# Performance work log

Hardware: AMD Instinct MI355X
Metric: run time of the kernel (lower is better)

The kernel has to match this reference:

```python
import jax, jax.numpy as jnp
import numpy as np

B, N, DIM, H, DH = 32, 1024, 512, 8, 64
SCALE = DH ** -0.5


def setup_inputs() -> dict:
    key = jax.random.key(0)
    k1, k2, k3, k4 = jax.random.split(key, 4)
    x = jax.random.normal(k1, (B, N, DIM), dtype=jnp.float32)
    W_qkv = jax.random.normal(k2, (DIM, 3 * H * DH), dtype=jnp.float32) * (DIM ** -0.5)
    W_out = jax.random.normal(k3, (H * DH, DIM), dtype=jnp.float32) * ((H * DH) ** -0.5)
    b_out = jnp.zeros((DIM,), dtype=jnp.float32)
    decay_mask = jax.random.uniform(k4, (1, H, N, N), dtype=jnp.float32)
    return {"x": x, "W_qkv": W_qkv, "W_out": W_out, "b_out": b_out,
            "decay_mask": decay_mask}


def reference(x, W_qkv, W_out, b_out, decay_mask):
    b, n, _ = x.shape
    qkv = x @ W_qkv                                  # [b, n, 3*h*d]
    q, k, v = jnp.split(qkv, 3, axis=-1)
    reshape = lambda t: t.reshape(b, n, H, DH).transpose(0, 2, 1, 3)  # b h n d
    q, k, v = reshape(q), reshape(k), reshape(v)
    dots = jnp.einsum('bhid,bhjd->bhij', q, k) * SCALE
    attn = jax.nn.softmax(dots, axis=-1)
    attn = attn * decay_mask                          # post-softmax decay mask
    out = jnp.einsum('bhij,bhjd->bhid', attn, v)      # [b, h, n, d]
    out = out.transpose(0, 2, 1, 3).reshape(b, n, H * DH)
    return out @ W_out + b_out
```

## Files before the change

### kernel.cpp

```cpp
#include <hip/hip_runtime.h>
#include <hip/hip_fp16.h>
#include <math.h>

#define Bb 32
#define Nn 1024
#define DIMc 512
#define Hh 8
#define DHd 64
#define GK 512

typedef __attribute__((ext_vector_type(8))) short short8;
typedef __attribute__((ext_vector_type(8))) _Float16 half8;
typedef __attribute__((ext_vector_type(2))) __fp16 fp16x2;
typedef __attribute__((ext_vector_type(4))) float floatx4;

#define MFMA16 __builtin_amdgcn_mfma_f32_16x16x32_f16

#if __has_builtin(__builtin_amdgcn_exp2f)
#define EXP2(x) __builtin_amdgcn_exp2f(x)
#else
#define EXP2(x) __expf((x) * 0.6931471805599453f)
#endif

__device__ __forceinline__ unsigned short f16_bits(float f) {
    return __half_as_ushort(__float2half(f));
}
__device__ __forceinline__ int cvt_pk_f16(float a, float b) {
    fp16x2 r = __builtin_amdgcn_cvt_pkrtz(a, b);
    return __builtin_bit_cast(int, r);
}

__global__ __launch_bounds__(256) void transpose_half_kernel(
    const float* __restrict__ src, int K, int N,
    unsigned short* __restrict__ dh)
{
    __shared__ float T[32][33];
    const int tid = threadIdx.x;
    const int c = tid & 31, r0 = tid >> 5;
    const int nb = blockIdx.x * 32, kb = blockIdx.y * 32;
    #pragma unroll
    for (int i = 0; i < 4; ++i)
        T[r0 + i * 8][c] = src[(size_t)(kb + r0 + i * 8) * N + nb + c];
    __syncthreads();
    #pragma unroll
    for (int i = 0; i < 4; ++i) {
        int n = r0 + i * 8;
        dh[(size_t)(nb + n) * K + kb + c] = f16_bits(T[c][n]);
    }
}

__global__ __launch_bounds__(256) void decay_to_half_kernel(
    const float* __restrict__ D, unsigned short* __restrict__ D16)
{
    size_t i = ((size_t)blockIdx.x * 256 + threadIdx.x) * 4;
    float4 v = *(const float4*)(D + i);
    ushort4 o;
    o.x = f16_bits(v.x * 0.00390625f);
    o.y = f16_bits(v.y * 0.00390625f);
    o.z = f16_bits(v.z * 0.00390625f);
    o.w = f16_bits(v.w * 0.00390625f);
    *(ushort4*)(D16 + i) = o;
}

__global__ __launch_bounds__(256) void x_to_half_kernel(
    const float* __restrict__ X, unsigned short* __restrict__ Xf)
{
    size_t i = ((size_t)blockIdx.x * 256 + threadIdx.x) * 8;
    float4 a = *(const float4*)(X + i);
    float4 b = *(const float4*)(X + i + 4);
    float f[8] = {a.x, a.y, a.z, a.w, b.x, b.y, b.z, b.w};
    short8 o;
    #pragma unroll
    for (int e = 0; e < 8; ++e) o[e] = (short)f16_bits(f[e]);
    *(short8*)(Xf + i) = o;
}

__device__ __forceinline__ void gload_lds16(const unsigned short* g, unsigned short* l) {
    __builtin_amdgcn_global_load_lds(
        (const __attribute__((address_space(1))) unsigned int*)g,
        (__attribute__((address_space(3))) unsigned int*)l,
        16, 0, 0);
}

#define STAGE2(PA, PB, k0s, bufp) do {                                         \
    _Pragma("unroll")                                                          \
    for (int i_ = 0; i_ < 2; ++i_) {                                           \
        const int row_ = i_ * 64 + w * 16 + l16;                               \
        const size_t aoff_ = (size_t)(m0 + row_) * GK + (k0s) + quad * 8;      \
        const size_t boff_ = (size_t)(n0 + row_) * GK + (k0s) + quad * 8;      \
        const int lbe_ = (i_ * 4 + w) * 512;                                   \
        gload_lds16((PA) + aoff_, (bufp) + lbe_);                              \
        gload_lds16((PB) + boff_, (bufp) + 4096 + lbe_);                       \
    }                                                                          \
} while (0)

__global__ __launch_bounds__(256) void gemm_qkv_mfma(
    const unsigned short* __restrict__ Xf, const unsigned short* __restrict__ Wf,
    unsigned short* __restrict__ Qf, unsigned short* __restrict__ Kf,
    unsigned short* __restrict__ Vt)
{
    __shared__ union {
        unsigned short buf[3][8192];
        unsigned short bounce[128][136];
    } u;

    const int tid  = threadIdx.x;
    const int w    = tid >> 6;
    const int lane = tid & 63;
    const int quad = lane >> 4;
    const int l16  = lane & 15;
    const int lb = blockIdx.x;
    const int wg = (lb & 7) * 384 + (lb >> 3);
    const int n0 = (wg % 12) * 128;
    const int m0 = (wg / 12) * 128;
    const int wm = w >> 1, wn = w & 1;

    floatx4 acc[4][4];
    #pragma unroll
    for (int im = 0; im < 4; ++im)
        #pragma unroll
        for (int in = 0; in < 4; ++in)
            acc[im][in] = (floatx4){0.f, 0.f, 0.f, 0.f};

    STAGE2(Xf, Wf, 0, u.buf[0]);
    STAGE2(Xf, Wf, 32, u.buf[1]);

    int rd = 0;
    for (int k0 = 0; k0 < GK; k0 += 32) {
        asm volatile("s_waitcnt vmcnt(4) lgkmcnt(0)" ::: "memory");
        __builtin_amdgcn_s_barrier();
        __builtin_amdgcn_sched_barrier(0);
        const int wr = (rd >= 1) ? rd - 1 : 2;
        STAGE2(Xf, Wf, k0 + 64, u.buf[wr]);

        const unsigned short* rp = u.buf[rd];
        half8 faf[4], fbf[4];
        #pragma unroll
        for (int t = 0; t < 4; ++t) {
            const int ca = ((wm * 4 + t) * 4 + quad) * 16 + l16;
            faf[t] = *(const half8*)&rp[ca * 8];
            const int cb = ((wn * 4 + t) * 4 + quad) * 16 + l16;
            fbf[t] = *(const half8*)&rp[4096 + cb * 8];
        }
        #pragma unroll
        for (int im = 0; im < 4; ++im)
            #pragma unroll
            for (int in = 0; in < 4; ++in)
                acc[im][in] = MFMA16(faf[im], fbf[in], acc[im][in], 0, 0, 0);
        rd = (rd == 2) ? 0 : rd + 1;
    }
    asm volatile("s_waitcnt vmcnt(0)" ::: "memory");

    const int which = n0 >> 9;
    const int b    = m0 >> 10;
    const int tokb = m0 & 1023;
    if (which < 2) {
        unsigned short* OUT = which ? Kf : Qf;
        const float sc = which ? 1.0f : 0.18033688011112042f;
        #pragma unroll
        for (int im = 0; im < 4; ++im) {
            const int tok = tokb + wm * 64 + im * 16 + quad * 4;
            #pragma unroll
            for (int in = 0; in < 4; ++in) {
                const int ncol = n0 + wn * 64 + in * 16 + l16;
                const int h = (ncol & 511) >> 6, d = ncol & 63;
                const size_t base = ((size_t)(b * Hh + h) * Nn + tok) * DHd + d;
                #pragma unroll
                for (int r = 0; r < 4; ++r)
                    OUT[base + (size_t)r * DHd] = f16_bits(acc[im][in][r] * sc);
            }
        }
    } else {
        __syncthreads();
        #pragma unroll
        for (int im = 0; im < 4; ++im)
            #pragma unroll
            for (int in = 0; in < 4; ++in)
                #pragma unroll
                for (int r = 0; r < 4; ++r)
                    u.bounce[wm * 64 + im * 16 + quad * 4 + r][wn * 64 + in * 16 + l16] =
                        f16_bits(acc[im][in][r]);
        __syncthreads();
        const int c = tid >> 1, tq = (tid & 1) * 64;
        const int h = ((n0 + c) & 511) >> 6, d = c & 63;
        unsigned short* vbase = Vt + ((size_t)(b * Hh + h) * DHd + d) * Nn + tokb;
        #pragma unroll
        for (int uu = 0; uu < 8; ++uu) {
            short8 v8;
            #pragma unroll
            for (int e = 0; e < 8; ++e)
                v8[e] = (short)u.bounce[tq + uu * 8 + e][c];
            *(short8*)&vbase[tq + uu * 8] = v8;
        }
    }
}

__global__ __launch_bounds__(256) void attn_mfma_kernel(
    const unsigned short* __restrict__ Qf, const unsigned short* __restrict__ Kf,
    const unsigned short* __restrict__ Vt, const unsigned short* __restrict__ D16,
    unsigned short* __restrict__ AOf)
{
    __shared__ unsigned short Kfs[2][32][72];
    __shared__ unsigned short Vts[2][64][40];

    const int tid  = threadIdx.x;
    const int wave = tid >> 6;
    const int lane = tid & 63;
    const int quad = lane >> 4;
    const int l16  = lane & 15;
    const int lb   = blockIdx.x;
    const int xcd  = lb & 7;
    const int r_   = lb >> 3;
    const int h    = r_ >> 5;
    const int rem  = r_ & 31;
    const int i0   = (rem >> 2) << 7;
    const int b    = xcd * 4 + (rem & 3);
    const int bh   = b * 8 + h;
    const int iw   = i0 + wave * 32;

    const size_t qoffA = ((size_t)bh * Nn + iw + l16) * DHd + quad * 8;
    const size_t qoffB = qoffA + (size_t)16 * DHd;
    const half8 qA0 = *(const half8*)(Qf + qoffA);
    const half8 qA1 = *(const half8*)(Qf + qoffA + 32);
    const half8 qB0 = *(const half8*)(Qf + qoffB);
    const half8 qB1 = *(const half8*)(Qf + qoffB + 32);

    floatx4 oA[4], oB[4];
    #pragma unroll
    for (int nt = 0; nt < 4; ++nt) {
        oA[nt] = (floatx4){0.f, 0.f, 0.f, 0.f};
        oB[nt] = (floatx4){0.f, 0.f, 0.f, 0.f};
    }
    float lA = 0.f, lB = 0.f;

    const int sj  = tid >> 3, sc2 = (tid & 7) * 8;
    const int prow = ((sj >> 2) & 1) * 16 + ((sj >> 3) << 2) + (sj & 3);
    const int vd  = tid >> 2, vj8 = (tid & 3) * 8;
    const unsigned short* DpA = D16 + ((size_t)h * Nn + iw + l16) * Nn + quad * 8;
    const unsigned short* DpB = DpA + (size_t)16 * Nn;

    const unsigned short* kpf = Kf + (size_t)bh * Nn * DHd + (size_t)sj * DHd + sc2;
    const unsigned short* vpv = Vt + (size_t)bh * DHd * Nn + (size_t)vd * Nn + vj8;

    short8 pk_f = *(const short8*)kpf; kpf += 32 * DHd;
    short8 pk_v = *(const short8*)vpv; vpv += 32;
    *(short8*)&Kfs[0][prow][sc2] = pk_f;
    *(short8*)&Vts[0][vd][vj8]   = pk_v;
    __syncthreads();

    int cur = 0;
    for (int j0 = 0; j0 < Nn; j0 += 32) {
        pk_f = *(const short8*)kpf; kpf += 32 * DHd;
        pk_v = *(const short8*)vpv; vpv += 32;
        const short8 dcA = *(const short8*)(DpA + j0);
        const short8 dcB = *(const short8*)(DpB + j0);

        floatx4 sA[2], sB[2];
        #pragma unroll
        for (int nh = 0; nh < 2; ++nh) {
            const int kr = nh * 16 + l16;
            half8 kf0 = *(const half8*)&Kfs[cur][kr][quad * 8];
            half8 kf1 = *(const half8*)&Kfs[cur][kr][32 + quad * 8];
            floatx4 a = (floatx4){0.f, 0.f, 0.f, 0.f};
            a = MFMA16(kf0, qA0, a, 0, 0, 0);
            a = MFMA16(kf1, qA1, a, 0, 0, 0);
            sA[nh] = a;
            floatx4 c = (floatx4){0.f, 0.f, 0.f, 0.f};
            c = MFMA16(kf0, qB0, c, 0, 0, 0);
            c = MFMA16(kf1, qB1, c, 0, 0, 0);
            sB[nh] = c;
        }

        float pA[8], pB[8];
        #pragma unroll
        for (int e = 0; e < 4; ++e) {
            pA[e]     = EXP2(sA[0][e]);
            pA[4 + e] = EXP2(sA[1][e]);
            pB[e]     = EXP2(sB[0][e]);
            pB[4 + e] = EXP2(sB[1][e]);
        }
        lA += ((pA[0] + pA[1]) + (pA[2] + pA[3])) + ((pA[4] + pA[5]) + (pA[6] + pA[7]));
        lB += ((pB[0] + pB[1]) + (pB[2] + pB[3])) + ((pB[4] + pB[5]) + (pB[6] + pB[7]));

        union { int i4[4]; half8 v8; } pfA, pfB;
        const int* dA = (const int*)&dcA;
        const int* dB = (const int*)&dcB;
        #pragma unroll
        for (int e = 0; e < 4; ++e) {
            fp16x2 pa = __builtin_bit_cast(fp16x2, cvt_pk_f16(pA[2 * e], pA[2 * e + 1]));
            fp16x2 da = __builtin_bit_cast(fp16x2, dA[e]);
            pfA.i4[e] = __builtin_bit_cast(int, pa * da);
            fp16x2 pb = __builtin_bit_cast(fp16x2, cvt_pk_f16(pB[2 * e], pB[2 * e + 1]));
            fp16x2 db = __builtin_bit_cast(fp16x2, dB[e]);
            pfB.i4[e] = __builtin_bit_cast(int, pb * db);
        }
        #pragma unroll
        for (int nt = 0; nt < 4; ++nt) {
            half8 vf = *(const half8*)&Vts[cur][nt * 16 + l16][quad * 8];
            oA[nt] = MFMA16(pfA.v8, vf, oA[nt], 0, 0, 0);
            oB[nt] = MFMA16(pfB.v8, vf, oB[nt], 0, 0, 0);
        }

        *(short8*)&Kfs[cur ^ 1][prow][sc2] = pk_f;
        *(short8*)&Vts[cur ^ 1][vd][vj8]   = pk_v;
        __syncthreads();
        cur ^= 1;
    }

    float lsA = lA;
    lsA += __shfl_xor(lsA, 16);
    lsA += __shfl_xor(lsA, 32);
    float lsB = lB;
    lsB += __shfl_xor(lsB, 16);
    lsB += __shfl_xor(lsB, 32);
    const float invA = 256.f / lsA;
    const float invB = 256.f / lsB;
    float irA[4], irB[4];
    #pragma unroll
    for (int r = 0; r < 4; ++r) {
        irA[r] = __shfl(invA, quad * 4 + r);
        irB[r] = __shfl(invB, quad * 4 + r);
    }
    const size_t aobA = ((size_t)b * Nn + iw) * DIMc + h * DHd;
    const size_t aobB = aobA + (size_t)16 * DIMc;
    #pragma unroll
    for (int nt = 0; nt < 4; ++nt)
        #pragma unroll
        for (int r = 0; r < 4; ++r) {
            const size_t ro = (size_t)(quad * 4 + r) * DIMc + nt * 16 + l16;
            AOf[aobA + ro] = f16_bits(oA[nt][r] * irA[r]);
            AOf[aobB + ro] = f16_bits(oB[nt][r] * irB[r]);
        }
}

__global__ __launch_bounds__(256) void gemm_out_mfma(
    const unsigned short* __restrict__ Af, const unsigned short* __restrict__ Wf,
    const float* __restrict__ bias, float* __restrict__ C)
{
    __shared__ unsigned short sbuf[3][8192];

    const int tid  = threadIdx.x;
    const int w    = tid >> 6;
    const int lane = tid & 63;
    const int quad = lane >> 4;
    const int l16  = lane & 15;
    const int lb = blockIdx.x;
    const int wg = (lb & 7) * 128 + (lb >> 3);
    const int n0 = (wg & 3) * 128;
    const int m0 = (wg >> 2) * 128;
    const int wm = w >> 1, wn = w & 1;

    floatx4 acc[4][4];
    #pragma unroll
    for (int im = 0; im < 4; ++im)
        #pragma unroll
        for (int in = 0; in < 4; ++in)
            acc[im][in] = (floatx4){0.f, 0.f, 0.f, 0.f};

    STAGE2(Af, Wf, 0, sbuf[0]);
    STAGE2(Af, Wf, 32, sbuf[1]);

    int rd = 0;
    for (int k0 = 0; k0 < GK; k0 += 32) {
        asm volatile("s_waitcnt vmcnt(4) lgkmcnt(0)" ::: "memory");
        __builtin_amdgcn_s_barrier();
        __builtin_amdgcn_sched_barrier(0);
        const int wr = (rd >= 1) ? rd - 1 : 2;
        STAGE2(Af, Wf, k0 + 64, sbuf[wr]);

        const unsigned short* rp = sbuf[rd];
        half8 faf[4], fbf[4];
        #pragma unroll
        for (int t = 0; t < 4; ++t) {
            const int ca = ((wm * 4 + t) * 4 + quad) * 16 + l16;
            faf[t] = *(const half8*)&rp[ca * 8];
            const int cb = ((wn * 4 + t) * 4 + quad) * 16 + l16;
            fbf[t] = *(const half8*)&rp[4096 + cb * 8];
        }
        #pragma unroll
        for (int im = 0; im < 4; ++im)
            #pragma unroll
            for (int in = 0; in < 4; ++in)
                acc[im][in] = MFMA16(faf[im], fbf[in], acc[im][in], 0, 0, 0);
        rd = (rd == 2) ? 0 : rd + 1;
    }
    asm volatile("s_waitcnt vmcnt(0)" ::: "memory");

    float biasv[4];
    #pragma unroll
    for (int in = 0; in < 4; ++in) biasv[in] = bias[n0 + wn * 64 + in * 16 + l16];
    #pragma unroll
    for (int im = 0; im < 4; ++im)
        #pragma unroll
        for (int in = 0; in < 4; ++in) {
            const int mrow = m0 + wm * 64 + im * 16 + quad * 4;
            const int ncol = n0 + wn * 64 + in * 16 + l16;
            #pragma unroll
            for (int r = 0; r < 4; ++r)
                C[(size_t)(mrow + r) * DIMc + ncol] = acc[im][in][r] + biasv[in];
        }
}

extern "C" void kernel_launch(void* const* d_in, const int* in_sizes, int n_in,
                              void* d_out, int out_size, void* d_ws, size_t ws_size,
                              hipStream_t stream)
{
    const float* x     = (const float*)d_in[0];
    const float* Wqkv  = (const float*)d_in[1];
    const float* Wout  = (const float*)d_in[2];
    const float* bout  = (const float*)d_in[3];
    const float* decay = (const float*)d_in[4];

    const size_t E = (size_t)32768 * 512;
    unsigned short* p = (unsigned short*)d_ws;
    unsigned short* Qf  = p; p += E;
    unsigned short* Kf  = p; p += E;
    unsigned short* Vt  = p; p += E;
    unsigned short* AOf = p; p += E;
    unsigned short* Wq  = p; p += 786432;
    unsigned short* Wo  = p; p += 262144;
    unsigned short* D16 = p;
    unsigned short* Xf = AOf;

    transpose_half_kernel<<<dim3(48, 16), 256, 0, stream>>>(Wqkv, 512, 1536, Wq);
    transpose_half_kernel<<<dim3(16, 16), 256, 0, stream>>>(Wout, 512, 512, Wo);
    decay_to_half_kernel<<<dim3(8192), 256, 0, stream>>>(decay, D16);
    x_to_half_kernel<<<dim3(8192), 256, 0, stream>>>(x, Xf);
    gemm_qkv_mfma<<<dim3(3072), 256, 0, stream>>>(Xf, Wq, Qf, Kf, Vt);
    attn_mfma_kernel<<<dim3(2048), 256, 0, stream>>>(Qf, Kf, Vt, D16, AOf);
    gemm_out_mfma<<<dim3(1024), 256, 0, stream>>>(AOf, Wo, bout, (float*)d_out);
}
```

Measured before the change: 293.7 us.

## Load GEMM operands straight from global memory into registers, bypassing LDS staging

Both MFMA GEMMs (the QKV projection and the output projection) drop the triple-buffered global-to-LDS staging with per-step barriers. Each wave now loads its A and B fragments directly from global memory into registers, double-buffered across two 32-wide K steps. This removes the LDS traffic and the block-wide barriers, frees shared memory (which may raise occupancy), and removes one __syncthreads before the V transpose bounce. In exchange, operand tiles are no longer shared between waves through LDS, so each tile is fetched twice through the caches. The final prefetch also reads 64 elements past the end of the K range, which is unused but goes out of bounds on the last row.

```diff
diff --git a/kernel.cpp b/kernel.cpp
--- a/kernel.cpp
+++ b/kernel.cpp
@@ -75,34 +75,12 @@
     *(short8*)(Xf + i) = o;
 }
 
-__device__ __forceinline__ void gload_lds16(const unsigned short* g, unsigned short* l) {
-    __builtin_amdgcn_global_load_lds(
-        (const __attribute__((address_space(1))) unsigned int*)g,
-        (__attribute__((address_space(3))) unsigned int*)l,
-        16, 0, 0);
-}
-
-#define STAGE2(PA, PB, k0s, bufp) do {                                         \
-    _Pragma("unroll")                                                          \
-    for (int i_ = 0; i_ < 2; ++i_) {                                           \
-        const int row_ = i_ * 64 + w * 16 + l16;                               \
-        const size_t aoff_ = (size_t)(m0 + row_) * GK + (k0s) + quad * 8;      \
-        const size_t boff_ = (size_t)(n0 + row_) * GK + (k0s) + quad * 8;      \
-        const int lbe_ = (i_ * 4 + w) * 512;                                   \
-        gload_lds16((PA) + aoff_, (bufp) + lbe_);                              \
-        gload_lds16((PB) + boff_, (bufp) + 4096 + lbe_);                       \
-    }                                                                          \
-} while (0)
-
 __global__ __launch_bounds__(256) void gemm_qkv_mfma(
     const unsigned short* __restrict__ Xf, const unsigned short* __restrict__ Wf,
     unsigned short* __restrict__ Qf, unsigned short* __restrict__ Kf,
     unsigned short* __restrict__ Vt)
 {
-    __shared__ union {
-        unsigned short buf[3][8192];
-        unsigned short bounce[128][136];
-    } u;
+    __shared__ unsigned short bounce[128][136];
 
     const int tid  = threadIdx.x;
     const int w    = tid >> 6;
@@ -122,34 +100,37 @@
         for (int in = 0; in < 4; ++in)
             acc[im][in] = (floatx4){0.f, 0.f, 0.f, 0.f};
 
-    STAGE2(Xf, Wf, 0, u.buf[0]);
-    STAGE2(Xf, Wf, 32, u.buf[1]);
-
-    int rd = 0;
-    for (int k0 = 0; k0 < GK; k0 += 32) {
-        asm volatile("s_waitcnt vmcnt(4) lgkmcnt(0)" ::: "memory");
-        __builtin_amdgcn_s_barrier();
-        __builtin_amdgcn_sched_barrier(0);
-        const int wr = (rd >= 1) ? rd - 1 : 2;
-        STAGE2(Xf, Wf, k0 + 64, u.buf[wr]);
-
-        const unsigned short* rp = u.buf[rd];
-        half8 faf[4], fbf[4];
+    const unsigned short* ap = Xf + (size_t)(m0 + wm * 64 + l16) * GK + quad * 8;
+    const unsigned short* bp = Wf + (size_t)(n0 + wn * 64 + l16) * GK + quad * 8;
+
+    half8 aC[4], bC[4], aN[4], bN[4];
+    #pragma unroll
+    for (int t = 0; t < 4; ++t) {
+        aC[t] = *(const half8*)(ap + (size_t)t * 16 * GK);
+        bC[t] = *(const half8*)(bp + (size_t)t * 16 * GK);
+    }
+    for (int k0 = 0; k0 < GK; k0 += 64) {
         #pragma unroll
         for (int t = 0; t < 4; ++t) {
-            const int ca = ((wm * 4 + t) * 4 + quad) * 16 + l16;
-            faf[t] = *(const half8*)&rp[ca * 8];
-            const int cb = ((wn * 4 + t) * 4 + quad) * 16 + l16;
-            fbf[t] = *(const half8*)&rp[4096 + cb * 8];
+            aN[t] = *(const half8*)(ap + (size_t)t * 16 * GK + k0 + 32);
+            bN[t] = *(const half8*)(bp + (size_t)t * 16 * GK + k0 + 32);
         }
         #pragma unroll
         for (int im = 0; im < 4; ++im)
             #pragma unroll
             for (int in = 0; in < 4; ++in)
-                acc[im][in] = MFMA16(faf[im], fbf[in], acc[im][in], 0, 0, 0);
-        rd = (rd == 2) ? 0 : rd + 1;
-    }
-    asm volatile("s_waitcnt vmcnt(0)" ::: "memory");
+                acc[im][in] = MFMA16(aC[im], bC[in], acc[im][in], 0, 0, 0);
+        #pragma unroll
+        for (int t = 0; t < 4; ++t) {
+            aC[t] = *(const half8*)(ap + (size_t)t * 16 * GK + k0 + 64);
+            bC[t] = *(const half8*)(bp + (size_t)t * 16 * GK + k0 + 64);
+        }
+        #pragma unroll
+        for (int im = 0; im < 4; ++im)
+            #pragma unroll
+            for (int in = 0; in < 4; ++in)
+                acc[im][in] = MFMA16(aN[im], bN[in], acc[im][in], 0, 0, 0);
+    }
 
     const int which = n0 >> 9;
     const int b    = m0 >> 10;
@@ -171,14 +152,13 @@
             }
         }
     } else {
-        __syncthreads();
         #pragma unroll
         for (int im = 0; im < 4; ++im)
             #pragma unroll
             for (int in = 0; in < 4; ++in)
                 #pragma unroll
                 for (int r = 0; r < 4; ++r)
-                    u.bounce[wm * 64 + im * 16 + quad * 4 + r][wn * 64 + in * 16 + l16] =
+                    bounce[wm * 64 + im * 16 + quad * 4 + r][wn * 64 + in * 16 + l16] =
                         f16_bits(acc[im][in][r]);
         __syncthreads();
         const int c = tid >> 1, tq = (tid & 1) * 64;
@@ -189,7 +169,7 @@
             short8 v8;
             #pragma unroll
             for (int e = 0; e < 8; ++e)
-                v8[e] = (short)u.bounce[tq + uu * 8 + e][c];
+                v8[e] = (short)bounce[tq + uu * 8 + e][c];
             *(short8*)&vbase[tq + uu * 8] = v8;
         }
     }
@@ -337,8 +317,6 @@
     const unsigned short* __restrict__ Af, const unsigned short* __restrict__ Wf,
     const float* __restrict__ bias, float* __restrict__ C)
 {
-    __shared__ unsigned short sbuf[3][8192];
-
     const int tid  = threadIdx.x;
     const int w    = tid >> 6;
     const int lane = tid & 63;
@@ -357,34 +335,37 @@
         for (int in = 0; in < 4; ++in)
             acc[im][in] = (floatx4){0.f, 0.f, 0.f, 0.f};
 
-    STAGE2(Af, Wf, 0, sbuf[0]);
-    STAGE2(Af, Wf, 32, sbuf[1]);
-
-    int rd = 0;
-    for (int k0 = 0; k0 < GK; k0 += 32) {
-        asm volatile("s_waitcnt vmcnt(4) lgkmcnt(0)" ::: "memory");
-        __builtin_amdgcn_s_barrier();
-        __builtin_amdgcn_sched_barrier(0);
-        const int wr = (rd >= 1) ? rd - 1 : 2;
-        STAGE2(Af, Wf, k0 + 64, sbuf[wr]);
-
-        const unsigned short* rp = sbuf[rd];
-        half8 faf[4], fbf[4];
+    const unsigned short* ap = Af + (size_t)(m0 + wm * 64 + l16) * GK + quad * 8;
+    const unsigned short* bp = Wf + (size_t)(n0 + wn * 64 + l16) * GK + quad * 8;
+
+    half8 aC[4], bC[4], aN[4], bN[4];
+    #pragma unroll
+    for (int t = 0; t < 4; ++t) {
+        aC[t] = *(const half8*)(ap + (size_t)t * 16 * GK);
+        bC[t] = *(const half8*)(bp + (size_t)t * 16 * GK);
+    }
+    for (int k0 = 0; k0 < GK; k0 += 64) {
         #pragma unroll
         for (int t = 0; t < 4; ++t) {
-            const int ca = ((wm * 4 + t) * 4 + quad) * 16 + l16;
-            faf[t] = *(const half8*)&rp[ca * 8];
-            const int cb = ((wn * 4 + t) * 4 + quad) * 16 + l16;
-            fbf[t] = *(const half8*)&rp[4096 + cb * 8];
+            aN[t] = *(const half8*)(ap + (size_t)t * 16 * GK + k0 + 32);
+            bN[t] = *(const half8*)(bp + (size_t)t * 16 * GK + k0 + 32);
         }
         #pragma unroll
         for (int im = 0; im < 4; ++im)
             #pragma unroll
             for (int in = 0; in < 4; ++in)
-                acc[im][in] = MFMA16(faf[im], fbf[in], acc[im][in], 0, 0, 0);
-        rd = (rd == 2) ? 0 : rd + 1;
-    }
-    asm volatile("s_waitcnt vmcnt(0)" ::: "memory");
+                acc[im][in] = MFMA16(aC[im], bC[in], acc[im][in], 0, 0, 0);
+        #pragma unroll
+        for (int t = 0; t < 4; ++t) {
+            aC[t] = *(const half8*)(ap + (size_t)t * 16 * GK + k0 + 64);
+            bC[t] = *(const half8*)(bp + (size_t)t * 16 * GK + k0 + 64);
+        }
+        #pragma unroll
+        for (int im = 0; im < 4; ++im)
+            #pragma unroll
+            for (int in = 0; in < 4; ++in)
+                acc[im][in] = MFMA16(aN[im], bN[in], acc[im][in], 0, 0, 0);
+    }
 
     float biasv[4];
     #pragma unroll
```

After: 405.7 us. 1.38x slower.
